# Optimization experiments

Hardware: AMD Instinct MI355X
Metric: run time of the kernel (lower is better)

Reference implementation:

```python
import jax, jax.numpy as jnp
import numpy as np

MARGIN = 0.3
NUM_CLASSES = 1000


def setup_inputs() -> dict:
    key = jax.random.key(0)
    k1, k2 = jax.random.split(key)
    B, D = 8192, 256
    inputs = jax.random.normal(k1, (B, D), dtype=jnp.float32)
    targets = jax.random.randint(k2, (B,), 0, NUM_CLASSES, dtype=jnp.int64)
    return {"inputs": inputs, "targets": targets}


def reference(inputs, targets):
    # Squared Euclidean pairwise distances: ||x_i||^2 + ||x_j||^2 - 2 x_i.x_j
    sq = jnp.sum(inputs * inputs, axis=1)                      # [B]
    dist = sq[:, None] + sq[None, :] - 2.0 * (inputs @ inputs.T)  # [B, B]

    # Hard mining: per-row max over positives (same label, incl. self),
    # min over negatives, exactly as the torch per-row masked max/min loop.
    pos_mask = targets[:, None] == targets[None, :]            # [B, B] bool
    neg_inf = jnp.float32(-jnp.inf)
    pos_inf = jnp.float32(jnp.inf)
    dist_ap = jnp.max(jnp.where(pos_mask, dist, neg_inf), axis=1)  # [B]
    dist_an = jnp.min(jnp.where(pos_mask, pos_inf, dist), axis=1)  # [B]

    # MarginRankingLoss(margin)(dist_an, dist_ap, y=1) = mean relu(ap - an + m)
    loss = jnp.mean(jax.nn.relu(dist_ap - dist_an + MARGIN))
    prec = jnp.mean((dist_an > dist_ap).astype(jnp.float32))
    return (loss, prec)
```

## Files before the change

kernel.cpp:

```cpp
#include <hip/hip_runtime.h>
#include <hip/hip_bf16.h>

#define B_N 8192
#define D_K 256
#define MARGIN 0.3f
#define NPAN 64

typedef float f32x4 __attribute__((ext_vector_type(4)));
typedef short s16x8 __attribute__((ext_vector_type(8)));

__device__ __forceinline__ void load_lds16(const unsigned short* g,
                                           unsigned short* l) {
    __builtin_amdgcn_global_load_lds(
        (const __attribute__((address_space(1))) unsigned int*)g,
        (__attribute__((address_space(3))) unsigned int*)l, 16, 0, 0);
}

__global__ __launch_bounds__(256) void prep_kernel(const float* __restrict__ X,
        float* __restrict__ sq, unsigned short* __restrict__ Xp,
        float* __restrict__ acc2) {
    int row  = (blockIdx.x << 2) + (threadIdx.x >> 6);
    int lane = threadIdx.x & 63;
    const float4 v = reinterpret_cast<const float4*>(X + (size_t)row * D_K)[lane];

    float xs[4] = {v.x, v.y, v.z, v.w};
    ushort4 hv;
    unsigned short* hp = &hv.x;
    float s = 0.f;
    #pragma unroll
    for (int i = 0; i < 4; ++i) {
        __hip_bfloat16 h = __float2bfloat16(xs[i]);
        hp[i] = *reinterpret_cast<unsigned short*>(&h);
        float hf = __bfloat162float(h);
        s = fmaf(hf, hf, s);
    }
    *reinterpret_cast<ushort4*>(Xp + (size_t)row * D_K + lane * 4) = hv;

    #pragma unroll
    for (int o = 32; o > 0; o >>= 1) s += __shfl_down(s, o, 64);
    if (lane == 0) sq[row] = s;
    if (blockIdx.x == 0 && threadIdx.x == 0) {
        acc2[0] = 0.f; acc2[1] = 0.f;
        reinterpret_cast<unsigned*>(acc2)[2] = 0u;
    }
}

#define BM 128
#define BN 128

__global__ __launch_bounds__(256, 4) void dist_kernel(
        const unsigned short* __restrict__ Xp,
        const int* __restrict__ tgt, const float* __restrict__ sq,
        float* __restrict__ part_ap, float* __restrict__ part_an) {
    __shared__ unsigned short Atile[128 * 64];
    __shared__ unsigned short Btile[128 * 64];
    __shared__ float rowap[128], rowan[128], colap[128], colan[128];

    const int t    = threadIdx.x;
    const int lane = t & 63;
    const int wave = t >> 6;
    const int wrow = (wave >> 1) * 64;
    const int wcol = (wave & 1) * 64;
    const int fr   = lane & 15;
    const int quad = lane >> 4;
    const float INF = __int_as_float(0x7f800000);

    int tt = blockIdx.x;
    int bx = (int)((sqrtf(8.f * (float)tt + 1.f) - 1.f) * 0.5f);
    while ((bx + 1) * (bx + 2) / 2 <= tt) ++bx;
    while (bx * (bx + 1) / 2 > tt) --bx;
    int by = tt - bx * (bx + 1) / 2;
    const int bm = by * BM;
    const int bn = bx * BN;

    const unsigned short* ag[4];
    const unsigned short* bg[4];
    unsigned short* al[4];
    unsigned short* bl[4];
    #pragma unroll
    for (int j = 0; j < 4; ++j) {
        int g = wave * 64 + j * 256 + lane;
        int r = g >> 3, s0 = g & 7;
        int u = s0 ^ (r & 7);
        ag[j] = Xp + (size_t)(bm + r) * D_K + u * 8;
        bg[j] = Xp + (size_t)(bn + r) * D_K + u * 8;
        al[j] = Atile + g * 8;
        bl[j] = Btile + g * 8;
    }

    f32x4 acc[4][4];
    #pragma unroll
    for (int i = 0; i < 4; ++i)
        #pragma unroll
        for (int j = 0; j < 4; ++j) acc[i][j] = (f32x4){0.f, 0.f, 0.f, 0.f};

    #pragma unroll 1
    for (int win = 0; win < 4; ++win) {
        __syncthreads();
        const int wo = win * 64;
        #pragma unroll
        for (int j = 0; j < 4; ++j) {
            load_lds16(ag[j] + wo, al[j]);
            load_lds16(bg[j] + wo, bl[j]);
        }
        __syncthreads();

        s16x8 a[4][2], b[4][2];
        #pragma unroll
        for (int mi = 0; mi < 4; ++mi) {
            int rb = (wrow + mi * 16 + fr) * 64;
            #pragma unroll
            for (int h = 0; h < 2; ++h) {
                int s = (h * 4 + quad) ^ (fr & 7);
                a[mi][h] = *reinterpret_cast<const s16x8*>(&Atile[rb + s * 8]);
            }
        }
        #pragma unroll
        for (int ni = 0; ni < 4; ++ni) {
            int rb = (wcol + ni * 16 + fr) * 64;
            #pragma unroll
            for (int h = 0; h < 2; ++h) {
                int s = (h * 4 + quad) ^ (fr & 7);
                b[ni][h] = *reinterpret_cast<const s16x8*>(&Btile[rb + s * 8]);
            }
        }
        #pragma unroll
        for (int mi = 0; mi < 4; ++mi)
            #pragma unroll
            for (int ni = 0; ni < 4; ++ni) {
                acc[mi][ni] = __builtin_amdgcn_mfma_f32_16x16x32_bf16(
                    a[mi][0], b[ni][0], acc[mi][ni], 0, 0, 0);
                acc[mi][ni] = __builtin_amdgcn_mfma_f32_16x16x32_bf16(
                    a[mi][1], b[ni][1], acc[mi][ni], 0, 0, 0);
            }
    }

    int   ct[4]; float csq[4];
    #pragma unroll
    for (int ni = 0; ni < 4; ++ni) {
        int c = bn + wcol + ni * 16 + fr;
        ct[ni] = tgt[c]; csq[ni] = sq[c];
    }
    float cap[4], can[4];
    #pragma unroll
    for (int ni = 0; ni < 4; ++ni) { cap[ni] = -INF; can[ni] = INF; }

    float rapv[16], ranv[16];
    #pragma unroll
    for (int mi = 0; mi < 4; ++mi) {
        #pragma unroll
        for (int reg = 0; reg < 4; ++reg) {
            int rl = wrow + mi * 16 + quad * 4 + reg;
            int rt = tgt[bm + rl]; float rsq = sq[bm + rl];
            float rap = -INF, ran = INF;
            #pragma unroll
            for (int ni = 0; ni < 4; ++ni) {
                float d = rsq + csq[ni] - 2.f * acc[mi][ni][reg];
                bool pos = (rt == ct[ni]);
                if (pos) { rap = fmaxf(rap, d); cap[ni] = fmaxf(cap[ni], d); }
                else     { ran = fminf(ran, d); can[ni] = fminf(can[ni], d); }
            }
            #pragma unroll
            for (int o = 1; o < 16; o <<= 1) {
                rap = fmaxf(rap, __shfl_xor(rap, o, 64));
                ran = fminf(ran, __shfl_xor(ran, o, 64));
            }
            rapv[mi * 4 + reg] = rap;
            ranv[mi * 4 + reg] = ran;
            if ((wave & 1) == 0 && fr == 0) {
                rowap[rl] = rap; rowan[rl] = ran;
            }
        }
    }

    #pragma unroll
    for (int ni = 0; ni < 4; ++ni) {
        #pragma unroll
        for (int o = 16; o < 64; o <<= 1) {
            cap[ni] = fmaxf(cap[ni], __shfl_xor(cap[ni], o, 64));
            can[ni] = fminf(can[ni], __shfl_xor(can[ni], o, 64));
        }
    }
    if (wave < 2 && lane < 16) {
        #pragma unroll
        for (int ni = 0; ni < 4; ++ni) {
            int c = wcol + ni * 16 + lane;
            colap[c] = cap[ni]; colan[c] = can[ni];
        }
    }

    __syncthreads();

    if (wave & 1) {
        #pragma unroll
        for (int mi = 0; mi < 4; ++mi)
            #pragma unroll
            for (int reg = 0; reg < 4; ++reg) {
                int rl = wrow + mi * 16 + quad * 4 + reg;
                if (fr == 0) {
                    part_ap[(size_t)bx * B_N + bm + rl] =
                        fmaxf(rapv[mi * 4 + reg], rowap[rl]);
                    part_an[(size_t)bx * B_N + bm + rl] =
                        fminf(ranv[mi * 4 + reg], rowan[rl]);
                }
            }
    }
    if (wave >= 2 && bx != by && lane < 16) {
        #pragma unroll
        for (int ni = 0; ni < 4; ++ni) {
            int c = wcol + ni * 16 + lane;
            part_ap[(size_t)by * B_N + bn + c] = fmaxf(cap[ni], colap[c]);
            part_an[(size_t)by * B_N + bn + c] = fminf(can[ni], colan[c]);
        }
    }
}

__global__ __launch_bounds__(256) void final_kernel(
        const float* __restrict__ part_ap, const float* __restrict__ part_an,
        float* __restrict__ acc2, float* __restrict__ out) {
    __shared__ float s_sum[4], s_cnt[4];
    int gid = blockIdx.x * 256 + threadIdx.x;
    int i   = gid >> 2;
    int qg  = gid & 3;
    const float* pa = part_ap + (size_t)(qg * 16) * B_N + i;
    const float* pn = part_an + (size_t)(qg * 16) * B_N + i;
    float ap = pa[0];
    float an = pn[0];
    #pragma unroll
    for (int k = 1; k < 16; ++k) {
        ap = fmaxf(ap, pa[(size_t)k * B_N]);
        an = fminf(an, pn[(size_t)k * B_N]);
    }
    #pragma unroll
    for (int o = 1; o < 4; o <<= 1) {
        ap = fmaxf(ap, __shfl_xor(ap, o, 64));
        an = fminf(an, __shfl_xor(an, o, 64));
    }
    float sum = 0.f, cnt = 0.f;
    if (qg == 0) {
        float v = ap - an + MARGIN;
        sum = v > 0.f ? v : 0.f;
        cnt = an > ap ? 1.f : 0.f;
    }
    #pragma unroll
    for (int o = 32; o > 0; o >>= 1) {
        sum += __shfl_down(sum, o, 64);
        cnt += __shfl_down(cnt, o, 64);
    }
    int wave = threadIdx.x >> 6, lane = threadIdx.x & 63;
    if (lane == 0) { s_sum[wave] = sum; s_cnt[wave] = cnt; }
    __syncthreads();
    if (threadIdx.x == 0) {
        float ts = 0.f, tc = 0.f;
        #pragma unroll
        for (int w = 0; w < 4; ++w) { ts += s_sum[w]; tc += s_cnt[w]; }
        atomicAdd(&acc2[0], ts);
        atomicAdd(&acc2[1], tc);
        __threadfence();
        unsigned ticket = atomicAdd(reinterpret_cast<unsigned*>(acc2) + 2, 1u);
        if (ticket == gridDim.x - 1) {
            float fs = atomicAdd(&acc2[0], 0.f);
            float fc = atomicAdd(&acc2[1], 0.f);
            out[0] = fs / (float)B_N;
            out[1] = fc / (float)B_N;
        }
    }
}

extern "C" void kernel_launch(void* const* d_in, const int* in_sizes, int n_in,
                              void* d_out, int out_size, void* d_ws, size_t ws_size,
                              hipStream_t stream) {
    const float* X   = (const float*)d_in[0];
    const int*   tgt = (const int*)d_in[1];

    char* ws = (char*)d_ws;
    float*          sq      = (float*)ws;
    float*          acc2    = (float*)(ws + 32768);
    float*          part_ap = (float*)(ws + 65536);
    float*          part_an = (float*)(ws + 65536 + 2097152);
    unsigned short* Xp      = (unsigned short*)(ws + 65536 + 4194304);

    float* out = (float*)d_out;

    prep_kernel<<<B_N / 4, 256, 0, stream>>>(X, sq, Xp, acc2);
    dist_kernel<<<(64 * 65) / 2, 256, 0, stream>>>(Xp, tgt, sq, part_ap, part_an);
    final_kernel<<<B_N / 64, 256, 0, stream>>>(part_ap, part_an, acc2, out);
}
```

Before: 113.3 us.

## Replace row shuffle reductions with padded LDS transpose and remap tile order

Per-row max/min partials are written to a padded shared-memory array that aliases the GEMM tile buffers. One thread per row then reduces the 32 partials, replacing the 16-lane butterfly shuffles and the rowap/rowan handoff between waves. Block indices are also permuted ((tt&7)*260 + tt>>3) so that consecutive blocks land on different XCDs or in a different traversal order, which may change L2 locality. The cost is an extra barrier before the epilogue and serial 32-element LDS reductions per row.

```diff
diff --git a/kernel.cpp b/kernel.cpp
--- a/kernel.cpp
+++ b/kernel.cpp
@@ -52,9 +52,12 @@
         const unsigned short* __restrict__ Xp,
         const int* __restrict__ tgt, const float* __restrict__ sq,
         float* __restrict__ part_ap, float* __restrict__ part_an) {
-    __shared__ unsigned short Atile[128 * 64];
-    __shared__ unsigned short Btile[128 * 64];
-    __shared__ float rowap[128], rowan[128], colap[128], colan[128];
+    __shared__ __align__(16) unsigned char uni[33792];
+    __shared__ float colap[128], colan[128];
+    unsigned short* Atile = reinterpret_cast<unsigned short*>(uni);
+    unsigned short* Btile = reinterpret_cast<unsigned short*>(uni + 16384);
+    float* APs = reinterpret_cast<float*>(uni);
+    float* ANs = reinterpret_cast<float*>(uni + 16896);
 
     const int t    = threadIdx.x;
     const int lane = t & 63;
@@ -66,6 +69,7 @@
     const float INF = __int_as_float(0x7f800000);
 
     int tt = blockIdx.x;
+    tt = (tt & 7) * 260 + (tt >> 3);
     int bx = (int)((sqrtf(8.f * (float)tt + 1.f) - 1.f) * 0.5f);
     while ((bx + 1) * (bx + 2) / 2 <= tt) ++bx;
     while (bx * (bx + 1) / 2 > tt) --bx;
@@ -135,6 +139,8 @@
             }
     }
 
+    __syncthreads();
+
     int   ct[4]; float csq[4];
     #pragma unroll
     for (int ni = 0; ni < 4; ++ni) {
@@ -145,7 +151,7 @@
     #pragma unroll
     for (int ni = 0; ni < 4; ++ni) { cap[ni] = -INF; can[ni] = INF; }
 
-    float rapv[16], ranv[16];
+    const int mcol = (wave & 1) * 16 + fr;
     #pragma unroll
     for (int mi = 0; mi < 4; ++mi) {
         #pragma unroll
@@ -160,16 +166,8 @@
                 if (pos) { rap = fmaxf(rap, d); cap[ni] = fmaxf(cap[ni], d); }
                 else     { ran = fminf(ran, d); can[ni] = fminf(can[ni], d); }
             }
-            #pragma unroll
-            for (int o = 1; o < 16; o <<= 1) {
-                rap = fmaxf(rap, __shfl_xor(rap, o, 64));
-                ran = fminf(ran, __shfl_xor(ran, o, 64));
-            }
-            rapv[mi * 4 + reg] = rap;
-            ranv[mi * 4 + reg] = ran;
-            if ((wave & 1) == 0 && fr == 0) {
-                rowap[rl] = rap; rowan[rl] = ran;
-            }
+            APs[rl * 33 + mcol] = rap;
+            ANs[rl * 33 + mcol] = ran;
         }
     }
 
@@ -191,20 +189,24 @@
 
     __syncthreads();
 
-    if (wave & 1) {
-        #pragma unroll
-        for (int mi = 0; mi < 4; ++mi)
-            #pragma unroll
-            for (int reg = 0; reg < 4; ++reg) {
-                int rl = wrow + mi * 16 + quad * 4 + reg;
-                if (fr == 0) {
-                    part_ap[(size_t)bx * B_N + bm + rl] =
-                        fmaxf(rapv[mi * 4 + reg], rowap[rl]);
-                    part_an[(size_t)bx * B_N + bm + rl] =
-                        fminf(ranv[mi * 4 + reg], rowan[rl]);
-                }
-            }
-    }
+    {
+        int arr = t >> 7;
+        int row = t & 127;
+        if (arr == 0) {
+            const float* p = APs + row * 33;
+            float v = p[0];
+            #pragma unroll
+            for (int j = 1; j < 32; ++j) v = fmaxf(v, p[j]);
+            part_ap[(size_t)bx * B_N + bm + row] = v;
+        } else {
+            const float* p = ANs + row * 33;
+            float v = p[0];
+            #pragma unroll
+            for (int j = 1; j < 32; ++j) v = fminf(v, p[j]);
+            part_an[(size_t)bx * B_N + bm + row] = v;
+        }
+    }
+
     if (wave >= 2 && bx != by && lane < 16) {
         #pragma unroll
         for (int ni = 0; ni < 4; ++ni) {
```

Result: faster. 102.7 us (-9.4%).
